# Kernel tuning notes

Measured on AMD Instinct MI355X. Metric: run time of the kernel, lower is better.

The kernel has to match this reference:

```python
import jax, jax.numpy as jnp
import numpy as np

N_NODES = 10000
N_EDGES = 100000
C = 64          # in_channels == out_channels (required by x_i + x_m)
D_EDGE = 16     # edge_attr feature dim


def setup_inputs() -> dict:
    key = jax.random.key(0)
    k_x, k_ei, k_ea, k_w, k_b, k_r, k_bias = jax.random.split(key, 7)
    x = jax.random.normal(k_x, (N_NODES, C), dtype=jnp.float32)
    edge_index = jax.random.randint(k_ei, (2, N_EDGES), 0, N_NODES, dtype=jnp.int32)
    edge_attr = jax.random.normal(k_ea, (N_EDGES, D_EDGE), dtype=jnp.float32)
    # nn = Linear(D_EDGE -> C*C), producing per-edge [C, C] weight matrices
    W_nn = jax.random.normal(k_w, (D_EDGE, C * C), dtype=jnp.float32) * (1.0 / np.sqrt(D_EDGE))
    b_nn = jax.random.normal(k_b, (C * C,), dtype=jnp.float32) * 0.01
    root = jax.random.normal(k_r, (C, C), dtype=jnp.float32) * (1.0 / np.sqrt(C))
    bias = jax.random.normal(k_bias, (C,), dtype=jnp.float32) * 0.01
    return {"x": x, "edge_index": edge_index, "edge_attr": edge_attr,
            "W_nn": W_nn, "b_nn": b_nn, "root": root, "bias": bias}


def reference(x, edge_index, edge_attr, W_nn, b_nn, root, bias):
    N, Cc = x.shape
    row, col = edge_index[0], edge_index[1]
    # per-edge weight matrices from nn(edge_attr): [E, C, C]
    e = (edge_attr @ W_nn + b_nn).reshape(-1, Cc, Cc)
    # gather source features and apply edge-conditioned matmul: [E, C]
    m = jnp.einsum('ec,eco->eo', x[row], e)
    # Faithful to torch loop: x_m[i] = m[col == i].mean() -> SCALAR mean over
    # all elements of incoming messages, broadcast across the feature row.
    seg_sum = jax.ops.segment_sum(m.sum(axis=1), col, num_segments=N)       # [N]
    cnt = jax.ops.segment_sum(jnp.ones_like(col, dtype=x.dtype), col,
                              num_segments=N) * Cc                            # [N]
    mean = jnp.where(cnt > 0, seg_sum / jnp.maximum(cnt, 1.0), 0.0)          # [N]
    x_m = jnp.broadcast_to(mean[:, None], (N, Cc))                            # [N, C]
    # root transform + bias
    out = x @ root + bias + x_m
    return out
```

## Files before the change

kernel.cpp:

```cpp
#include <hip/hip_runtime.h>
#include <hip/hip_bf16.h>


#define CC 64
#define DE 16
#define PAD 65
#define EBLK 256

__global__ __launch_bounds__(256) void k_edge_direct(const float* __restrict__ W,
                                                     const float* __restrict__ b,
                                                     const float* __restrict__ x,
                                                     const int* __restrict__ ei,
                                                     const float* __restrict__ ea,
                                                     float* __restrict__ seg,
                                                     float* __restrict__ cnt,
                                                     int E) {
    __shared__ float ws[1024 + CC];
    const int tid = threadIdx.x;

    for (int p = tid; p < 1024 + CC; p += 256) {
        const float4* src = (p < 1024) ? (const float4*)(W + (size_t)p * CC)
                                       : (const float4*)(b + (size_t)(p - 1024) * CC);
        float s = 0.f;
#pragma unroll
        for (int i = 0; i < 16; ++i) { float4 v = src[i]; s += v.x + v.y + v.z + v.w; }
        ws[p] = s;
    }
    __syncthreads();

    const float4* ws4 = (const float4*)ws;
    const float4* bs4 = (const float4*)(ws + 1024);

    for (int e = blockIdx.x * 256 + tid; e < E; e += EBLK * 256) {
        const int r  = ei[e];
        const int cn = ei[E + e];

        const float4* a4 = (const float4*)(ea + (size_t)e * DE);
        float4 av[4];
#pragma unroll
        for (int i = 0; i < 4; ++i) av[i] = a4[i];
        float eas[DE] = { av[0].x, av[0].y, av[0].z, av[0].w,
                          av[1].x, av[1].y, av[1].z, av[1].w,
                          av[2].x, av[2].y, av[2].z, av[2].w,
                          av[3].x, av[3].y, av[3].z, av[3].w };

        float4 u[16];
#pragma unroll
        for (int c4 = 0; c4 < 16; ++c4) u[c4] = bs4[c4];
#pragma unroll
        for (int d = 0; d < DE; ++d) {
            float ed = eas[d];
#pragma unroll
            for (int c4 = 0; c4 < 16; ++c4) {
                float4 w = ws4[d * 16 + c4];
                u[c4].x += ed * w.x; u[c4].y += ed * w.y;
                u[c4].z += ed * w.z; u[c4].w += ed * w.w;
            }
        }

        const float4* x4 = (const float4*)(x + (size_t)r * CC);
        float s = 0.f;
#pragma unroll
        for (int c4 = 0; c4 < 16; ++c4) {
            float4 xv = x4[c4];
            s += u[c4].x * xv.x + u[c4].y * xv.y + u[c4].z * xv.z + u[c4].w * xv.w;
        }

        atomicAdd(seg + cn, s);
        atomicAdd(cnt + cn, 1.0f);
    }
}

__global__ __launch_bounds__(256) void k_final(const float* __restrict__ x,
                                               const float* __restrict__ root,
                                               const float* __restrict__ bias,
                                               const float* __restrict__ seg,
                                               const float* __restrict__ cnt,
                                               float* __restrict__ out,
                                               int N) {
    __shared__ float rt[CC * CC];
    __shared__ float xs[16 * PAD];
    __shared__ float bi[CC];
    __shared__ float mn[16];
    int tid = threadIdx.x;
    int n0 = blockIdx.x * 16;

#pragma unroll
    for (int i = 0; i < 16; ++i) rt[tid + i * 256] = root[tid + i * 256];
#pragma unroll
    for (int it = 0; it < 4; ++it) {
        int i = it * 256 + tid;
        if ((size_t)n0 * CC + i < (size_t)N * CC)
            xs[(i >> 6) * PAD + (i & 63)] = x[(size_t)n0 * CC + i];
    }
    if (tid < CC) bi[tid] = bias[tid];
    if (tid < 16 && n0 + tid < N) {
        float c = cnt[n0 + tid];
        mn[tid] = c > 0.f ? seg[n0 + tid] / (c * (float)CC) : 0.f;
    }
    __syncthreads();

    int nl = tid >> 4, ci = tid & 15;
    int n = n0 + nl;
    if (n >= N) return;

    const float4* rt4 = (const float4*)rt;
    const float4* bi4 = (const float4*)bi;
    float m = mn[nl];
    float4 bv = bi4[ci];
    float4 acc = make_float4(bv.x + m, bv.y + m, bv.z + m, bv.w + m);
#pragma unroll
    for (int k = 0; k < CC; ++k) {
        float a  = xs[nl * PAD + k];
        float4 w = rt4[k * 16 + ci];
        acc.x += a * w.x; acc.y += a * w.y; acc.z += a * w.z; acc.w += a * w.w;
    }
    *(float4*)(out + (size_t)n * CC + ci * 4) = acc;
}

extern "C" void kernel_launch(void* const* d_in, const int* in_sizes, int n_in,
                              void* d_out, int out_size, void* d_ws, size_t ws_size,
                              hipStream_t stream) {
    const float* x    = (const float*)d_in[0];
    const int*   ei   = (const int*)  d_in[1];
    const float* ea   = (const float*)d_in[2];
    const float* W    = (const float*)d_in[3];
    const float* b    = (const float*)d_in[4];
    const float* root = (const float*)d_in[5];
    const float* bias = (const float*)d_in[6];
    float* out = (float*)d_out;
    float* ws  = (float*)d_ws;

    const int N = in_sizes[0] / CC;
    const int E = in_sizes[1] / 2;

    float* seg = ws;
    float* cnt = ws + N;

    int fBlocks = (N + 15) / 16;

    k_edge_direct<<<EBLK,    256, 0, stream>>>(W, b, x, ei, ea, seg, cnt, E);
    k_final      <<<fBlocks, 256, 0, stream>>>(x, root, bias, seg, cnt, out, N);
}
```

Baseline: 116.1 us.

## Replace global atomics with per-block LDS histograms and packed edge counts

Each of 128 blocks now handles a contiguous chunk of edges and accumulates message sums in a shared-memory histogram over all nodes. It adds a constant marker per edge so the edge count and the sum share one float slot, then writes the histogram to a per-block partial buffer. The final kernel reduces the 128 partials in double precision and decodes count and sum by rounding. This is meant to remove global atomic contention and the second count atomic, at the cost of writing and reading a partials array of about 5 MB. It also loses float precision from the large marker offset and hardcodes a node limit of 10240.

```diff
diff --git a/kernel.cpp b/kernel.cpp
--- a/kernel.cpp
+++ b/kernel.cpp
@@ -5,33 +5,41 @@
 #define CC 64
 #define DE 16
 #define PAD 65
-#define EBLK 256
+#define NPART 128
+#define HN 10240
+#define MARKF 65536.0f
+#define MARKD 65536.0
 
-__global__ __launch_bounds__(256) void k_edge_direct(const float* __restrict__ W,
-                                                     const float* __restrict__ b,
-                                                     const float* __restrict__ x,
-                                                     const int* __restrict__ ei,
-                                                     const float* __restrict__ ea,
-                                                     float* __restrict__ seg,
-                                                     float* __restrict__ cnt,
-                                                     int E) {
+__global__ __launch_bounds__(256) void k_edge_hist(const float* __restrict__ W,
+                                                   const float* __restrict__ b,
+                                                   const float* __restrict__ x,
+                                                   const int* __restrict__ ei,
+                                                   const float* __restrict__ ea,
+                                                   float* __restrict__ partial,
+                                                   int N, int E) {
     __shared__ float ws[1024 + CC];
+    __shared__ float hist[HN];
     const int tid = threadIdx.x;
+
+    for (int i = tid; i < HN; i += 256) hist[i] = 0.f;
 
     for (int p = tid; p < 1024 + CC; p += 256) {
         const float4* src = (p < 1024) ? (const float4*)(W + (size_t)p * CC)
                                        : (const float4*)(b + (size_t)(p - 1024) * CC);
-        float s = 0.f;
+        float v = 0.f;
 #pragma unroll
-        for (int i = 0; i < 16; ++i) { float4 v = src[i]; s += v.x + v.y + v.z + v.w; }
-        ws[p] = s;
+        for (int i = 0; i < 16; ++i) { float4 q = src[i]; v += q.x + q.y + q.z + q.w; }
+        ws[p] = v;
     }
     __syncthreads();
 
     const float4* ws4 = (const float4*)ws;
     const float4* bs4 = (const float4*)(ws + 1024);
 
-    for (int e = blockIdx.x * 256 + tid; e < E; e += EBLK * 256) {
+    const int chunk = (E + NPART - 1) / NPART;
+    const int e1 = min(E, (blockIdx.x + 1) * chunk);
+
+    for (int e = blockIdx.x * chunk + tid; e < e1; e += 256) {
         const int r  = ei[e];
         const int cn = ei[E + e];
 
@@ -66,16 +74,19 @@
             s += u[c4].x * xv.x + u[c4].y * xv.y + u[c4].z * xv.z + u[c4].w * xv.w;
         }
 
-        atomicAdd(seg + cn, s);
-        atomicAdd(cnt + cn, 1.0f);
+        atomicAdd(&hist[cn], s + MARKF);
     }
+    __syncthreads();
+
+    float4*       p4 = (float4*)(partial + (size_t)blockIdx.x * N);
+    const float4* h4 = (const float4*)hist;
+    for (int i = tid; i < N / 4; i += 256) p4[i] = h4[i];
 }
 
 __global__ __launch_bounds__(256) void k_final(const float* __restrict__ x,
                                                const float* __restrict__ root,
                                                const float* __restrict__ bias,
-                                               const float* __restrict__ seg,
-                                               const float* __restrict__ cnt,
+                                               const float* __restrict__ partial,
                                                float* __restrict__ out,
                                                int N) {
     __shared__ float rt[CC * CC];
@@ -94,9 +105,16 @@
             xs[(i >> 6) * PAD + (i & 63)] = x[(size_t)n0 * CC + i];
     }
     if (tid < CC) bi[tid] = bias[tid];
-    if (tid < 16 && n0 + tid < N) {
-        float c = cnt[n0 + tid];
-        mn[tid] = c > 0.f ? seg[n0 + tid] / (c * (float)CC) : 0.f;
+    if (tid < 16) {
+        int n = n0 + tid;
+        if (n < N) {
+            double t = 0.0;
+            for (int k = 0; k < NPART; ++k)
+                t += (double)partial[(size_t)k * N + n];
+            double c  = rint(t * (1.0 / MARKD));
+            float  sg = (float)(t - c * MARKD);
+            mn[tid] = c > 0.0 ? sg / ((float)c * (float)CC) : 0.f;
+        } else mn[tid] = 0.f;
     }
     __syncthreads();
 
@@ -134,11 +152,10 @@
     const int N = in_sizes[0] / CC;
     const int E = in_sizes[1] / 2;
 
-    float* seg = ws;
-    float* cnt = ws + N;
+    float* partial = ws;
 
     int fBlocks = (N + 15) / 16;
 
-    k_edge_direct<<<EBLK,    256, 0, stream>>>(W, b, x, ei, ea, seg, cnt, E);
-    k_final      <<<fBlocks, 256, 0, stream>>>(x, root, bias, seg, cnt, out, N);
+    k_edge_hist<<<NPART,  256, 0, stream>>>(W, b, x, ei, ea, partial, N, E);
+    k_final    <<<fBlocks, 256, 0, stream>>>(x, root, bias, partial, out, N);
 }
```

Measured after the change: 135.2 us. 1.16x slower.
